# Kernel optimization log

Hardware: AMD Instinct MI355X
Metric: run time of the kernel (lower is better)

## Reference

```python
import jax, jax.numpy as jnp
import numpy as np

D = 256           # input_dim
PROCESS_STEP = 4
N_SUPPORT = 512
BATCH = 32768


def setup_inputs() -> dict:
    key = jax.random.key(0)
    ks = jax.random.split(key, 8)
    H = 2 * D  # LSTMCell hidden size
    scale = 0.05
    return {
        "support_mean": jax.random.normal(ks[0], (N_SUPPORT, D), jnp.float32),
        "support_var": jax.random.uniform(ks[1], (N_SUPPORT, D), jnp.float32),
        "query_mean": jax.random.normal(ks[2], (BATCH, D), jnp.float32),
        "query_var": jax.random.uniform(ks[3], (BATCH, D), jnp.float32),
        # LSTMCell(D, 2D) parameters (PyTorch layout: [4*H, in] / [4*H, H])
        "W_ih": jax.random.normal(ks[4], (4 * H, D), jnp.float32) * scale,
        "W_hh": jax.random.normal(ks[5], (4 * H, H), jnp.float32) * scale,
        "b_ih": jax.random.normal(ks[6], (4 * H,), jnp.float32) * scale,
        "b_hh": jax.random.normal(ks[7], (4 * H,), jnp.float32) * scale,
    }


def _lstm_cell(x, h, c, W_ih, W_hh, b_ih, b_hh):
    # gates: [B, 4H], PyTorch gate order: input, forget, cell(g), output
    gates = x @ W_ih.T + b_ih + h @ W_hh.T + b_hh
    i, f, g, o = jnp.split(gates, 4, axis=1)
    i = jax.nn.sigmoid(i)
    f = jax.nn.sigmoid(f)
    g = jnp.tanh(g)
    o = jax.nn.sigmoid(o)
    c_new = f * c + i * g
    h_new = o * jnp.tanh(c_new)
    return h_new, c_new


def reference(support_mean, support_var, query_mean, query_var,
              W_ih, W_hh, b_ih, b_hh):
    # support_var / query_var are unused by the original forward.
    B = query_mean.shape[0]
    H = 2 * D
    h_r = jnp.zeros((B, H), query_mean.dtype)
    c = jnp.zeros((B, H), query_mean.dtype)
    h = query_mean  # placeholder; overwritten in first step
    for _ in range(PROCESS_STEP):
        h_r_, c = _lstm_cell(query_mean, h_r, c, W_ih, W_hh, b_ih, b_hh)
        h = query_mean + h_r_[:, :D]                       # [B, D]
        attn = jax.nn.softmax(h @ support_mean.T, axis=1)   # [B, S]
        r = attn @ support_mean                              # [B, D]
        h_r = jnp.concatenate((h, r), axis=1)                # [B, 2D]
    matching_scores = jnp.squeeze(h @ support_mean.T)        # [B, S]
    return matching_scores
```

## Files before the change

kernel.cpp:

```cpp
#include <hip/hip_runtime.h>

typedef unsigned int uint;
typedef unsigned short ushort;
typedef __attribute__((ext_vector_type(8))) short bhalf8;
typedef __attribute__((ext_vector_type(4))) float floatx4;

#define D_IN 256
#define NUNIT 256
#define GN 1024
#define NSUP 512
#define BATCH_N 32768
#define LDA_A 768

__device__ __forceinline__ ushort f2b(float f){
  union { float f; uint u; } x; x.f = f;
  uint r = (x.u + 0x7fffu + ((x.u >> 16) & 1u)) >> 16;
  return (ushort)r;
}
__device__ __forceinline__ float b2f(ushort u){
  union { uint u; float f; } x; x.u = ((uint)u) << 16;
  return x.f;
}
__device__ __forceinline__ float sigmf(float x){ return 1.0f / (1.0f + __expf(-x)); }
__device__ __forceinline__ float tanhfast(float x){ return 1.0f - 2.0f / (1.0f + __expf(2.0f * x)); }

__device__ __forceinline__ void stage_swz4(
    ushort* lds, const ushort* __restrict__ g, int ld, int row0, int k0,
    int wave, int lane)
{
  const int rsub = lane >> 3;
  const int oct  = (lane & 7) ^ rsub;
  #pragma unroll
  for (int q = 0; q < 4; q++) {
    const ushort* gp = g + (long)(row0 + wave * 32 + q * 8 + rsub) * ld
                         + k0 + (oct << 3);
    ushort* lp = lds + (wave * 32 + q * 8) * 64;
    __builtin_amdgcn_global_load_lds(
        (const __attribute__((address_space(1))) void*)gp,
        (__attribute__((address_space(3))) void*)lp, 16, 0, 0);
  }
}

__device__ __forceinline__ void stage_swz8(
    ushort* lds, const ushort* __restrict__ g, int ld, int row0, int k0,
    int wave, int lane)
{
  const int rsub = lane >> 3;
  const int oct  = (lane & 7) ^ rsub;
  #pragma unroll
  for (int q = 0; q < 2; q++) {
    const ushort* gp = g + (long)(row0 + wave * 16 + q * 8 + rsub) * ld
                         + k0 + (oct << 3);
    ushort* lp = lds + (wave * 16 + q * 8) * 64;
    __builtin_amdgcn_global_load_lds(
        (const __attribute__((address_space(1))) void*)gp,
        (__attribute__((address_space(3))) void*)lp, 16, 0, 0);
  }
}

__device__ __forceinline__ bhalf8 frag_ld(const ushort* lds, int R, int O, int sx)
{
  return *reinterpret_cast<const bhalf8*>(&lds[R * 64 + (((O ^ sx) & 7) << 3)]);
}

__device__ __forceinline__ bhalf8 frag_ld512(const ushort* lds, int R, int g, int O, int sx)
{
  return *reinterpret_cast<const bhalf8*>(&lds[R * 512 + g * 64 + (((O ^ sx) & 7) << 3)]);
}

__global__ __launch_bounds__(512) void gemm_gq_fused(
    const ushort* __restrict__ Qb,
    const ushort* __restrict__ Wq,
    const float4* __restrict__ biasp,
    uint2* __restrict__ Gq,
    float* __restrict__ cbuf,
    const float* __restrict__ query,
    ushort* __restrict__ Hhi,
    ushort* __restrict__ Hlo)
{
  __shared__ ushort SM[2][8192];

  const int tid  = threadIdx.x;
  const int lane = tid & 63;
  const int wave = tid >> 6;
  const int wrow = (wave >> 1) * 32;
  const int wcol = (wave & 1) * 64;
  const int wg = (blockIdx.x & 7) * (gridDim.x >> 3) + (blockIdx.x >> 3);
  const int bm = wg >> 3;
  const int bn = wg & 7;
  const int rowA0 = bm * 128;
  const int colB0 = bn * 128;

  floatx4 acc[2][4];
  #pragma unroll
  for (int m = 0; m < 2; m++)
    #pragma unroll
    for (int n = 0; n < 4; n++)
      acc[m][n] = (floatx4){0.f, 0.f, 0.f, 0.f};

  const int lr = lane & 15;
  const int lg = lane >> 4;
  const int sx = lane & 7;

  for (int k0 = 0; k0 < 256; k0 += 64) {
    stage_swz8(SM[0], Qb, 256, rowA0, k0, wave, lane);
    stage_swz8(SM[1], Wq, 256, colB0, k0, wave, lane);
    __syncthreads();
    #pragma unroll
    for (int ks = 0; ks < 2; ks++) {
      bhalf8 af[2], bfr[4];
      #pragma unroll
      for (int m = 0; m < 2; m++)
        af[m] = frag_ld(SM[0], wrow + m * 16 + lr, ks * 4 + lg, sx);
      #pragma unroll
      for (int n = 0; n < 4; n++)
        bfr[n] = frag_ld(SM[1], wcol + n * 16 + lr, ks * 4 + lg, sx);
      #pragma unroll
      for (int m = 0; m < 2; m++)
        #pragma unroll
        for (int n = 0; n < 4; n++)
          acc[m][n] = __builtin_amdgcn_mfma_f32_16x16x32_bf16(af[m], bfr[n], acc[m][n], 0, 0, 0);
    }
    __syncthreads();
  }

  ushort* ehi = (ushort*)SM[0];
  ushort* elo = ehi + 128 * 32;
  float*  ec  = (float*)SM[1];

  const int u_loc = (wave & 1) * 16 + lr;
  const int u     = bn * 32 + u_loc;
  const float4 b4 = biasp[u];
  #pragma unroll
  for (int m = 0; m < 2; m++) {
    #pragma unroll
    for (int rr = 0; rr < 4; rr++) {
      const int  rloc = wrow + m * 16 + lg * 4 + rr;
      const long row  = rowA0 + rloc;
      float pi = acc[m][0][rr] + b4.x;
      float pf = acc[m][1][rr] + b4.y;
      float pg = acc[m][2][rr] + b4.z;
      float po = acc[m][3][rr] + b4.w;
      uint2 pk;
      pk.x = (uint)f2b(pi) | ((uint)f2b(pf) << 16);
      pk.y = (uint)f2b(pg) | ((uint)f2b(po) << 16);
      Gq[row * NUNIT + u] = pk;
      float cn = sigmf(pi) * tanhfast(pg);
      ec[rloc * 32 + u_loc] = cn;
      float h = query[row * D_IN + u] + sigmf(po) * tanhfast(cn);
      ushort hh = f2b(h);
      ehi[rloc * 32 + u_loc] = hh;
      elo[rloc * 32 + u_loc] = f2b(h - b2f(hh));
    }
  }
  __syncthreads();
  const int u0 = bn * 32;
  {
    int row = tid >> 2, part = tid & 3;
    *(uint4*)(Hhi + (long)(rowA0 + row) * LDA_A + u0 + part * 8) = ((const uint4*)ehi)[tid];
    *(uint4*)(Hlo + (long)(rowA0 + row) * D_IN + u0 + part * 8) = ((const uint4*)elo)[tid];
  }
  #pragma unroll
  for (int i = tid; i < 1024; i += 512) {
    int row = i >> 3, part = i & 7;
    *(uint4*)(cbuf + (long)(rowA0 + row) * NUNIT + u0 + part * 4) = ((const uint4*)ec)[i];
  }
}

__global__ __launch_bounds__(512) void gemm_gates_fused(
    const ushort* __restrict__ A,
    const ushort* __restrict__ W,
    const uint2* __restrict__ Gq,
    float* __restrict__ cbuf,
    const float* __restrict__ query,
    ushort* __restrict__ Hhi,
    ushort* __restrict__ Hlo)
{
  __shared__ ushort SM[2][2][8192];

  const int tid  = threadIdx.x;
  const int lane = tid & 63;
  const int wave = tid >> 6;
  const int wrow = (wave >> 1) * 32;
  const int wcol = (wave & 1) * 64;
  const int wg = (blockIdx.x & 7) * (gridDim.x >> 3) + (blockIdx.x >> 3);
  const int bm = wg >> 3;
  const int bn = wg & 7;
  const int rowA0 = bm * 128;
  const int colB0 = bn * 128;

  floatx4 acc[2][4];
  #pragma unroll
  for (int m = 0; m < 2; m++)
    #pragma unroll
    for (int n = 0; n < 4; n++)
      acc[m][n] = (floatx4){0.f, 0.f, 0.f, 0.f};

  const int lr = lane & 15;
  const int lg = lane >> 4;
  const int sx = lane & 7;

  stage_swz8(SM[0][0], A, LDA_A, rowA0, 0, wave, lane);
  stage_swz8(SM[0][1], W, 512,   colB0, 0, wave, lane);
  __syncthreads();

  for (int t = 0; t < 8; t++) {
    const int cur = t & 1;
    if (t + 1 < 8) {
      stage_swz8(SM[cur ^ 1][0], A, LDA_A, rowA0, (t + 1) * 64, wave, lane);
      stage_swz8(SM[cur ^ 1][1], W, 512,   colB0, (t + 1) * 64, wave, lane);
    }
    const ushort* As = SM[cur][0];
    const ushort* Bs = SM[cur][1];
    #pragma unroll
    for (int ks = 0; ks < 2; ks++) {
      bhalf8 af[2], bfr[4];
      #pragma unroll
      for (int m = 0; m < 2; m++)
        af[m] = frag_ld(As, wrow + m * 16 + lr, ks * 4 + lg, sx);
      #pragma unroll
      for (int n = 0; n < 4; n++)
        bfr[n] = frag_ld(Bs, wcol + n * 16 + lr, ks * 4 + lg, sx);
      #pragma unroll
      for (int m = 0; m < 2; m++)
        #pragma unroll
        for (int n = 0; n < 4; n++)
          acc[m][n] = __builtin_amdgcn_mfma_f32_16x16x32_bf16(af[m], bfr[n], acc[m][n], 0, 0, 0);
    }
    __syncthreads();
  }

  ushort* ehi = (ushort*)SM[0][0];
  ushort* elo = ehi + 128 * 32;
  float*  ec  = (float*)SM[0][1];

  const int u_loc = (wave & 1) * 16 + lr;
  const int u     = bn * 32 + u_loc;
  #pragma unroll
  for (int m = 0; m < 2; m++) {
    #pragma unroll
    for (int rr = 0; rr < 4; rr++) {
      const int  rloc = wrow + m * 16 + lg * 4 + rr;
      const long row  = rowA0 + rloc;
      uint2 pk = Gq[row * NUNIT + u];
      float pi = acc[m][0][rr] + b2f((ushort)(pk.x & 0xffff));
      float pf = acc[m][1][rr] + b2f((ushort)(pk.x >> 16));
      float pg = acc[m][2][rr] + b2f((ushort)(pk.y & 0xffff));
      float po = acc[m][3][rr] + b2f((ushort)(pk.y >> 16));
      float cn = sigmf(pf) * cbuf[row * NUNIT + u] + sigmf(pi) * tanhfast(pg);
      ec[rloc * 32 + u_loc] = cn;
      float h = query[row * D_IN + u] + sigmf(po) * tanhfast(cn);
      ushort hh = f2b(h);
      ehi[rloc * 32 + u_loc] = hh;
      elo[rloc * 32 + u_loc] = f2b(h - b2f(hh));
    }
  }
  __syncthreads();
  const int u0 = bn * 32;
  {
    int row = tid >> 2, part = tid & 3;
    *(uint4*)(Hhi + (long)(rowA0 + row) * LDA_A + u0 + part * 8) = ((const uint4*)ehi)[tid];
    *(uint4*)(Hlo + (long)(rowA0 + row) * D_IN + u0 + part * 8) = ((const uint4*)elo)[tid];
  }
  #pragma unroll
  for (int i = tid; i < 1024; i += 512) {
    int row = i >> 3, part = i & 7;
    *(uint4*)(cbuf + (long)(rowA0 + row) * NUNIT + u0 + part * 4) = ((const uint4*)ec)[i];
  }
}

__global__ __launch_bounds__(256) void gemm_scores(
    const ushort* __restrict__ Ahi,
    const ushort* __restrict__ Alo,
    const ushort* __restrict__ Bhi, const ushort* __restrict__ Blo,
    float* __restrict__ C)
{
  __shared__ ushort AsH[128 * 64];
  __shared__ ushort AsL[128 * 64];
  __shared__ ushort BsH[128 * 64];
  __shared__ ushort BsL[128 * 64];

  const int tid  = threadIdx.x;
  const int lane = tid & 63;
  const int wave = tid >> 6;
  const int wr = (wave >> 1) * 64;
  const int wc = (wave & 1) * 64;
  const int wg = (blockIdx.x & 7) * (gridDim.x >> 3) + (blockIdx.x >> 3);
  const int bm = wg >> 2;
  const int bn = wg & 3;
  const int rowA0 = bm * 128;
  const int rowB0 = bn * 128;

  floatx4 acc[4][4];
  #pragma unroll
  for (int m = 0; m < 4; m++)
    #pragma unroll
    for (int n = 0; n < 4; n++)
      acc[m][n] = (floatx4){0.f, 0.f, 0.f, 0.f};

  const int lr = lane & 15;
  const int lg = lane >> 4;
  const int sx = lane & 7;

  for (int k0 = 0; k0 < D_IN; k0 += 64) {
    stage_swz4(AsH, Ahi, LDA_A, rowA0, k0, wave, lane);
    stage_swz4(AsL, Alo, D_IN,  rowA0, k0, wave, lane);
    stage_swz4(BsH, Bhi, D_IN,  rowB0, k0, wave, lane);
    stage_swz4(BsL, Blo, D_IN,  rowB0, k0, wave, lane);
    __syncthreads();
    #pragma unroll
    for (int ks = 0; ks < 2; ks++) {
      bhalf8 afh[4], afl[4], bfh[4], bfl[4];
      #pragma unroll
      for (int m = 0; m < 4; m++) {
        afh[m] = frag_ld(AsH, wr + m * 16 + lr, ks * 4 + lg, sx);
        afl[m] = frag_ld(AsL, wr + m * 16 + lr, ks * 4 + lg, sx);
      }
      #pragma unroll
      for (int n = 0; n < 4; n++) {
        bfh[n] = frag_ld(BsH, wc + n * 16 + lr, ks * 4 + lg, sx);
        bfl[n] = frag_ld(BsL, wc + n * 16 + lr, ks * 4 + lg, sx);
      }
      #pragma unroll
      for (int m = 0; m < 4; m++)
        #pragma unroll
        for (int n = 0; n < 4; n++) {
          acc[m][n] = __builtin_amdgcn_mfma_f32_16x16x32_bf16(afl[m], bfh[n], acc[m][n], 0, 0, 0);
          acc[m][n] = __builtin_amdgcn_mfma_f32_16x16x32_bf16(afh[m], bfl[n], acc[m][n], 0, 0, 0);
          acc[m][n] = __builtin_amdgcn_mfma_f32_16x16x32_bf16(afh[m], bfh[n], acc[m][n], 0, 0, 0);
        }
    }
    __syncthreads();
  }

  #pragma unroll
  for (int m = 0; m < 4; m++)
    #pragma unroll
    for (int n = 0; n < 4; n++)
      #pragma unroll
      for (int r = 0; r < 4; r++) {
        int row = rowA0 + wr + m * 16 + lg * 4 + r;
        int col = rowB0 + wc + n * 16 + lr;
        C[(long)row * NSUP + col] = acc[m][n][r];
      }
}

__global__ __launch_bounds__(512) void k_spv(
    const float* __restrict__ sc,
    const ushort* __restrict__ B,
    ushort* __restrict__ Cv)
{
  __shared__ ushort Ps[32 * 512];
  __shared__ ushort Bs[256 * 64];

  const int tid  = threadIdx.x;
  const int lane = tid & 63;
  const int wave = tid >> 6;
  const int wg = (blockIdx.x & 7) * (gridDim.x >> 3) + (blockIdx.x >> 3);
  const long rowA0 = (long)wg * 32;

  const int po  = (lane >> 1) & 7;
  const int ph4 = (lane & 1) * 4;
  const int pg0 = lane >> 4;
  #pragma unroll
  for (int j = 0; j < 4; j++) {
    const int r = wave * 4 + j;
    const float4* sp = reinterpret_cast<const float4*>(sc + (rowA0 + r) * NSUP);
    float4 v0 = sp[lane];
    float4 v1 = sp[64 + lane];
    float m = fmaxf(fmaxf(fmaxf(v0.x, v0.y), fmaxf(v0.z, v0.w)),
                    fmaxf(fmaxf(v1.x, v1.y), fmaxf(v1.z, v1.w)));
    #pragma unroll
    for (int off = 32; off >= 1; off >>= 1) m = fmaxf(m, __shfl_xor(m, off));
    float e0 = __expf(v0.x - m), e1 = __expf(v0.y - m), e2 = __expf(v0.z - m), e3 = __expf(v0.w - m);
    float e4 = __expf(v1.x - m), e5 = __expf(v1.y - m), e6 = __expf(v1.z - m), e7 = __expf(v1.w - m);
    float s = e0 + e1 + e2 + e3 + e4 + e5 + e6 + e7;
    #pragma unroll
    for (int off = 32; off >= 1; off >>= 1) s += __shfl_xor(s, off);
    float inv = 1.0f / s;
    uint2 p0, p1;
    p0.x = (uint)f2b(e0 * inv) | ((uint)f2b(e1 * inv) << 16);
    p0.y = (uint)f2b(e2 * inv) | ((uint)f2b(e3 * inv) << 16);
    p1.x = (uint)f2b(e4 * inv) | ((uint)f2b(e5 * inv) << 16);
    p1.y = (uint)f2b(e6 * inv) | ((uint)f2b(e7 * inv) << 16);
    const int os = ((po ^ (r & 7)) << 3) + ph4;
    *(uint2*)&Ps[r * 512 + (pg0    ) * 64 + os] = p0;
    *(uint2*)&Ps[r * 512 + (pg0 + 4) * 64 + os] = p1;
  }
  __syncthreads();

  floatx4 acc[2][2];
  #pragma unroll
  for (int m = 0; m < 2; m++)
    #pragma unroll
    for (int n = 0; n < 2; n++)
      acc[m][n] = (floatx4){0.f, 0.f, 0.f, 0.f};

  const int lr = lane & 15;
  const int lg = lane >> 4;
  const int sx = lane & 7;

  for (int kc = 0; kc < 8; kc++) {
    stage_swz4(Bs, B, NSUP, 0, kc * 64, wave, lane);
    __syncthreads();
    #pragma unroll
    for (int ks = 0; ks < 2; ks++) {
      bhalf8 af[2], bfr[2];
      #pragma unroll
      for (int m = 0; m < 2; m++)
        af[m] = frag_ld512(Ps, m * 16 + lr, kc, ks * 4 + lg, sx);
      #pragma unroll
      for (int n = 0; n < 2; n++)
        bfr[n] = frag_ld(Bs, wave * 32 + n * 16 + lr, ks * 4 + lg, sx);
      #pragma unroll
      for (int m = 0; m < 2; m++)
        #pragma unroll
        for (int n = 0; n < 2; n++)
          acc[m][n] = __builtin_amdgcn_mfma_f32_16x16x32_bf16(af[m], bfr[n], acc[m][n], 0, 0, 0);
    }
    __syncthreads();
  }

  ushort* elr = Ps;
  #pragma unroll
  for (int m = 0; m < 2; m++)
    #pragma unroll
    for (int n = 0; n < 2; n++)
      #pragma unroll
      for (int r = 0; r < 4; r++) {
        int rloc = m * 16 + lg * 4 + r;
        int cloc = wave * 32 + n * 16 + lr;
        elr[rloc * 256 + cloc] = f2b(acc[m][n][r]);
      }
  __syncthreads();
  #pragma unroll
  for (int i = tid; i < 1024; i += 512) {
    int row = i >> 5, part = i & 31;
    *(uint4*)(Cv + (rowA0 + row) * LDA_A + part * 8) = ((const uint4*)elr)[i];
  }
}

__global__ __launch_bounds__(256) void k_build(
    const float* __restrict__ Wih, const float* __restrict__ Whh,
    const float* __restrict__ bih, const float* __restrict__ bhh,
    const float* __restrict__ S,
    ushort* __restrict__ We, ushort* __restrict__ Wo, ushort* __restrict__ Wq,
    float4* __restrict__ biasp,
    ushort* __restrict__ Shi, ushort* __restrict__ Slo,
    ushort* __restrict__ STb)
{
  int t = blockIdx.x * 256 + threadIdx.x;
  if (t < GN * 512) {
    int c = t >> 9, k = t & 511;
    int unit = (c >> 6) * 16 + (c & 15);
    int gate = (c >> 4) & 3;
    long srow = (long)(gate * 512 + unit);
    We[(long)c * 512 + k] = f2b(Whh[srow * 512 + k]);
    int ko = (k < 256) ? (256 + k) : (k - 256);
    Wo[(long)c * 512 + k] = f2b(Whh[srow * 512 + ko]);
    if (k < 256) Wq[(long)c * 256 + k] = f2b(Wih[srow * 256 + k]);
  }
  if (t < NUNIT) {
    biasp[t] = make_float4(bih[t] + bhh[t],
                           bih[512 + t] + bhh[512 + t],
                           bih[1024 + t] + bhh[1024 + t],
                           bih[1536 + t] + bhh[1536 + t]);
  }
  if (t < NSUP * D_IN) {
    float v = S[t];
    ushort hv = f2b(v);
    Shi[t] = hv;
    Slo[t] = f2b(v - b2f(hv));
    int s = t >> 8, d = t & 255;
    STb[(long)d * NSUP + s] = hv;
  }
}

__global__ __launch_bounds__(256) void k_initq(
    const float* __restrict__ query, ushort* __restrict__ Qb)
{
  long t = (long)blockIdx.x * 256 + threadIdx.x;
  Qb[t] = f2b(query[t]);
}

extern "C" void kernel_launch(void* const* d_in, const int* in_sizes, int n_in,
                              void* d_out, int out_size, void* d_ws, size_t ws_size,
                              hipStream_t stream)
{
  const float* support_mean = (const float*)d_in[0];
  const float* query_mean   = (const float*)d_in[2];
  const float* W_ih = (const float*)d_in[4];
  const float* W_hh = (const float*)d_in[5];
  const float* b_ih = (const float*)d_in[6];
  const float* b_hh = (const float*)d_in[7];
  float* out = (float*)d_out;

  char* ws = (char*)d_ws;
  size_t off = 0;
  auto alloc = [&](size_t bytes) {
    void* p = ws + off;
    off += (bytes + 255) & ~(size_t)255;
    return p;
  };
  ushort* Abuf  = (ushort*)alloc((size_t)BATCH_N * LDA_A * 2);
  ushort* Qb    = (ushort*)alloc((size_t)BATCH_N * D_IN * 2);
  ushort* We    = (ushort*)alloc((size_t)GN * 512 * 2);
  ushort* Wo    = (ushort*)alloc((size_t)GN * 512 * 2);
  ushort* Wq    = (ushort*)alloc((size_t)GN * 256 * 2);
  float4* biasp = (float4*)alloc((size_t)NUNIT * 16);
  ushort* Shi   = (ushort*)alloc((size_t)NSUP * D_IN * 2);
  ushort* Slo   = (ushort*)alloc((size_t)NSUP * D_IN * 2);
  ushort* STb   = (ushort*)alloc((size_t)D_IN * NSUP * 2);
  float*  cbuf  = (float*) alloc((size_t)BATCH_N * NUNIT * 4);
  ushort* Hlo   = (ushort*)alloc((size_t)BATCH_N * D_IN * 2);
  uint2*  Gq    = (uint2*) alloc((size_t)BATCH_N * NUNIT * 8);
  if (off > ws_size) return;

  hipLaunchKernelGGL(k_build, dim3((GN * 512) / 256), dim3(256), 0, stream,
                     W_ih, W_hh, b_ih, b_hh, support_mean,
                     We, Wo, Wq, biasp, Shi, Slo, STb);
  hipLaunchKernelGGL(k_initq, dim3((BATCH_N * D_IN) / 256), dim3(256), 0, stream,
                     query_mean, Qb);

  hipLaunchKernelGGL(gemm_gq_fused,
                     dim3((BATCH_N / 128) * (GN / 128)), dim3(512), 0, stream,
                     Qb, Wq, biasp, Gq, cbuf, query_mean, Abuf + 0, Hlo);

  for (int s = 0; s < 4; s++) {
    const int hoff = (s & 1) * 512;
    hipLaunchKernelGGL(gemm_scores,
                       dim3((BATCH_N / 128) * (NSUP / 128)), dim3(256), 0, stream,
                       Abuf + hoff, Hlo, Shi, Slo, out);
    if (s < 3) {
      hipLaunchKernelGGL(k_spv, dim3(BATCH_N / 32), dim3(512), 0, stream,
                         out, STb, Abuf + 256);
      const int aoff = ((s + 1) == 2) ? 256 : 0;
      const ushort* Wnext = ((s + 1) == 2) ? Wo : We;
      hipLaunchKernelGGL(gemm_gates_fused,
                         dim3((BATCH_N / 128) * (GN / 128)), dim3(512), 0, stream,
                         Abuf + aoff, Wnext, Gq, cbuf, query_mean,
                         Abuf + ((s + 1) & 1) * 512, Hlo);
    }
  }
}
```

Measured before the change: 499.8 us.

## Fuse score GEMM, softmax and attention-value GEMM into one kernel

Replaces the separate scores GEMM plus softmax/PV kernel in the first three steps with a single kernel. Each 64-row block computes split-precision scores against the support set in LDS, applies softmax in place, and multiplies by the transposed support matrix. This removes the fp32 score matrix round trip through global memory (32768x512 floats written and read per step) and one launch per step. In exchange, each block reloads the full support matrix from global/L2 and uses 128KB of LDS, which limits occupancy to one block per CU.

```diff
diff --git a/kernel.cpp b/kernel.cpp
--- a/kernel.cpp
+++ b/kernel.cpp
@@ -24,38 +24,35 @@
 __device__ __forceinline__ float sigmf(float x){ return 1.0f / (1.0f + __expf(-x)); }
 __device__ __forceinline__ float tanhfast(float x){ return 1.0f - 2.0f / (1.0f + __expf(2.0f * x)); }
 
+__device__ __forceinline__ void stage_rows8(
+    ushort* lds_base, const ushort* __restrict__ g, int ld,
+    long grow0, int lrow0, int k0, int lane)
+{
+  const int rsub = lane >> 3;
+  const int oct  = (lane & 7) ^ rsub;
+  const ushort* gp = g + (grow0 + lrow0 + rsub) * ld + k0 + (oct << 3);
+  ushort* lp = lds_base + lrow0 * 64;
+  __builtin_amdgcn_global_load_lds(
+      (const __attribute__((address_space(1))) void*)gp,
+      (__attribute__((address_space(3))) void*)lp, 16, 0, 0);
+}
+
 __device__ __forceinline__ void stage_swz4(
     ushort* lds, const ushort* __restrict__ g, int ld, int row0, int k0,
     int wave, int lane)
 {
-  const int rsub = lane >> 3;
-  const int oct  = (lane & 7) ^ rsub;
-  #pragma unroll
-  for (int q = 0; q < 4; q++) {
-    const ushort* gp = g + (long)(row0 + wave * 32 + q * 8 + rsub) * ld
-                         + k0 + (oct << 3);
-    ushort* lp = lds + (wave * 32 + q * 8) * 64;
-    __builtin_amdgcn_global_load_lds(
-        (const __attribute__((address_space(1))) void*)gp,
-        (__attribute__((address_space(3))) void*)lp, 16, 0, 0);
-  }
+  #pragma unroll
+  for (int q = 0; q < 4; q++)
+    stage_rows8(lds, g, ld, row0, wave * 32 + q * 8, k0, lane);
 }
 
 __device__ __forceinline__ void stage_swz8(
     ushort* lds, const ushort* __restrict__ g, int ld, int row0, int k0,
     int wave, int lane)
 {
-  const int rsub = lane >> 3;
-  const int oct  = (lane & 7) ^ rsub;
-  #pragma unroll
-  for (int q = 0; q < 2; q++) {
-    const ushort* gp = g + (long)(row0 + wave * 16 + q * 8 + rsub) * ld
-                         + k0 + (oct << 3);
-    ushort* lp = lds + (wave * 16 + q * 8) * 64;
-    __builtin_amdgcn_global_load_lds(
-        (const __attribute__((address_space(1))) void*)gp,
-        (__attribute__((address_space(3))) void*)lp, 16, 0, 0);
-  }
+  #pragma unroll
+  for (int q = 0; q < 2; q++)
+    stage_rows8(lds, g, ld, row0, wave * 16 + q * 8, k0, lane);
 }
 
 __device__ __forceinline__ bhalf8 frag_ld(const ushort* lds, int R, int O, int sx)
@@ -345,96 +342,189 @@
       }
 }
 
-__global__ __launch_bounds__(512) void k_spv(
-    const float* __restrict__ sc,
-    const ushort* __restrict__ B,
+__global__ __launch_bounds__(512) void k_sspv(
+    const ushort* __restrict__ Ahi,
+    const ushort* __restrict__ Alo,
+    const ushort* __restrict__ Shi,
+    const ushort* __restrict__ Slo,
+    const ushort* __restrict__ STb,
     ushort* __restrict__ Cv)
 {
-  __shared__ ushort Ps[32 * 512];
-  __shared__ ushort Bs[256 * 64];
+  __shared__ ushort SMEM[65536];
+  ushort* Areg = SMEM;
+  ushort* Breg = SMEM + 32768;
 
   const int tid  = threadIdx.x;
   const int lane = tid & 63;
   const int wave = tid >> 6;
   const int wg = (blockIdx.x & 7) * (gridDim.x >> 3) + (blockIdx.x >> 3);
-  const long rowA0 = (long)wg * 32;
-
+  const long rowA0 = (long)wg * 64;
+
+  const int lr = lane & 15;
+  const int lg = lane >> 4;
+  const int sx = lane & 7;
+
+  {
+    const ushort* asrc = (wave < 4) ? Ahi : Alo;
+    const int ald = (wave < 4) ? LDA_A : D_IN;
+    ushort* adst = Areg + (wave >> 2) * 16384 + (wave & 3) * 4096;
+    const int ak0 = (wave & 3) * 64;
+    #pragma unroll
+    for (int q = 0; q < 8; q++)
+      stage_rows8(adst, asrc, ald, rowA0, q * 8, ak0, lane);
+  }
+  #pragma unroll
+  for (int q = 0; q < 8; q++)
+    stage_rows8(Breg, Shi, D_IN, 0, wave * 64 + q * 8, 0, lane);
+  __syncthreads();
+
+  floatx4 acc[4][4];
+  #pragma unroll
+  for (int m = 0; m < 4; m++)
+    #pragma unroll
+    for (int n = 0; n < 4; n++)
+      acc[m][n] = (floatx4){0.f, 0.f, 0.f, 0.f};
+
+  for (int kc = 0; kc < 4; kc++) {
+    const ushort* Ah = Areg + kc * 4096;
+    const ushort* Al = Areg + 16384 + kc * 4096;
+    #pragma unroll
+    for (int ks = 0; ks < 2; ks++) {
+      bhalf8 afh[4], afl[4], bfh[4];
+      #pragma unroll
+      for (int m = 0; m < 4; m++) {
+        afh[m] = frag_ld(Ah, m * 16 + lr, ks * 4 + lg, sx);
+        afl[m] = frag_ld(Al, m * 16 + lr, ks * 4 + lg, sx);
+      }
+      #pragma unroll
+      for (int n = 0; n < 4; n++)
+        bfh[n] = frag_ld(Breg, wave * 64 + n * 16 + lr, ks * 4 + lg, sx);
+      #pragma unroll
+      for (int m = 0; m < 4; m++)
+        #pragma unroll
+        for (int n = 0; n < 4; n++) {
+          acc[m][n] = __builtin_amdgcn_mfma_f32_16x16x32_bf16(afl[m], bfh[n], acc[m][n], 0, 0, 0);
+          acc[m][n] = __builtin_amdgcn_mfma_f32_16x16x32_bf16(afh[m], bfh[n], acc[m][n], 0, 0, 0);
+        }
+    }
+    __syncthreads();
+    #pragma unroll
+    for (int q = 0; q < 8; q++)
+      stage_rows8(Breg, Slo, D_IN, 0, wave * 64 + q * 8, kc * 64, lane);
+    __syncthreads();
+    #pragma unroll
+    for (int ks = 0; ks < 2; ks++) {
+      bhalf8 afh[4], bfl[4];
+      #pragma unroll
+      for (int m = 0; m < 4; m++)
+        afh[m] = frag_ld(Ah, m * 16 + lr, ks * 4 + lg, sx);
+      #pragma unroll
+      for (int n = 0; n < 4; n++)
+        bfl[n] = frag_ld(Breg, wave * 64 + n * 16 + lr, ks * 4 + lg, sx);
+      #pragma unroll
+      for (int m = 0; m < 4; m++)
+        #pragma unroll
+        for (int n = 0; n < 4; n++)
+          acc[m][n] = __builtin_amdgcn_mfma_f32_16x16x32_bf16(afh[m], bfl[n], acc[m][n], 0, 0, 0);
+    }
+    __syncthreads();
+    if (kc < 3) {
+      #pragma unroll
+      for (int q = 0; q < 8; q++)
+        stage_rows8(Breg, Shi, D_IN, 0, wave * 64 + q * 8, (kc + 1) * 64, lane);
+      __syncthreads();
+    }
+  }
+
+  float*  scf = (float*)Breg;
+  ushort* Ps  = Areg;
   const int po  = (lane >> 1) & 7;
   const int ph4 = (lane & 1) * 4;
   const int pg0 = lane >> 4;
-  #pragma unroll
-  for (int j = 0; j < 4; j++) {
-    const int r = wave * 4 + j;
-    const float4* sp = reinterpret_cast<const float4*>(sc + (rowA0 + r) * NSUP);
-    float4 v0 = sp[lane];
-    float4 v1 = sp[64 + lane];
-    float m = fmaxf(fmaxf(fmaxf(v0.x, v0.y), fmaxf(v0.z, v0.w)),
-                    fmaxf(fmaxf(v1.x, v1.y), fmaxf(v1.z, v1.w)));
-    #pragma unroll
-    for (int off = 32; off >= 1; off >>= 1) m = fmaxf(m, __shfl_xor(m, off));
-    float e0 = __expf(v0.x - m), e1 = __expf(v0.y - m), e2 = __expf(v0.z - m), e3 = __expf(v0.w - m);
-    float e4 = __expf(v1.x - m), e5 = __expf(v1.y - m), e6 = __expf(v1.z - m), e7 = __expf(v1.w - m);
-    float s = e0 + e1 + e2 + e3 + e4 + e5 + e6 + e7;
-    #pragma unroll
-    for (int off = 32; off >= 1; off >>= 1) s += __shfl_xor(s, off);
-    float inv = 1.0f / s;
-    uint2 p0, p1;
-    p0.x = (uint)f2b(e0 * inv) | ((uint)f2b(e1 * inv) << 16);
-    p0.y = (uint)f2b(e2 * inv) | ((uint)f2b(e3 * inv) << 16);
-    p1.x = (uint)f2b(e4 * inv) | ((uint)f2b(e5 * inv) << 16);
-    p1.y = (uint)f2b(e6 * inv) | ((uint)f2b(e7 * inv) << 16);
-    const int os = ((po ^ (r & 7)) << 3) + ph4;
-    *(uint2*)&Ps[r * 512 + (pg0    ) * 64 + os] = p0;
-    *(uint2*)&Ps[r * 512 + (pg0 + 4) * 64 + os] = p1;
-  }
-  __syncthreads();
-
-  floatx4 acc[2][2];
-  #pragma unroll
-  for (int m = 0; m < 2; m++)
+
+  #pragma unroll
+  for (int half = 0; half < 2; half++) {
+    #pragma unroll
+    for (int mm = 0; mm < 2; mm++) {
+      const int m = half * 2 + mm;
+      #pragma unroll
+      for (int n = 0; n < 4; n++)
+        #pragma unroll
+        for (int r = 0; r < 4; r++)
+          scf[(mm * 16 + lg * 4 + r) * 512 + wave * 64 + n * 16 + lr] = acc[m][n][r];
+    }
+    __syncthreads();
+    #pragma unroll
+    for (int j = 0; j < 4; j++) {
+      const int rl = wave * 4 + j;
+      const int r  = half * 32 + rl;
+      const float4* sp = reinterpret_cast<const float4*>(scf + rl * 512);
+      float4 v0 = sp[lane];
+      float4 v1 = sp[64 + lane];
+      float m = fmaxf(fmaxf(fmaxf(v0.x, v0.y), fmaxf(v0.z, v0.w)),
+                      fmaxf(fmaxf(v1.x, v1.y), fmaxf(v1.z, v1.w)));
+      #pragma unroll
+      for (int off = 32; off >= 1; off >>= 1) m = fmaxf(m, __shfl_xor(m, off));
+      float e0 = __expf(v0.x - m), e1 = __expf(v0.y - m), e2 = __expf(v0.z - m), e3 = __expf(v0.w - m);
+      float e4 = __expf(v1.x - m), e5 = __expf(v1.y - m), e6 = __expf(v1.z - m), e7 = __expf(v1.w - m);
+      float s = e0 + e1 + e2 + e3 + e4 + e5 + e6 + e7;
+      #pragma unroll
+      for (int off = 32; off >= 1; off >>= 1) s += __shfl_xor(s, off);
+      float inv = 1.0f / s;
+      uint2 p0, p1;
+      p0.x = (uint)f2b(e0 * inv) | ((uint)f2b(e1 * inv) << 16);
+      p0.y = (uint)f2b(e2 * inv) | ((uint)f2b(e3 * inv) << 16);
+      p1.x = (uint)f2b(e4 * inv) | ((uint)f2b(e5 * inv) << 16);
+      p1.y = (uint)f2b(e6 * inv) | ((uint)f2b(e7 * inv) << 16);
+      const int os = ((po ^ (r & 7)) << 3) + ph4;
+      *(uint2*)&Ps[r * 512 + (pg0    ) * 64 + os] = p0;
+      *(uint2*)&Ps[r * 512 + (pg0 + 4) * 64 + os] = p1;
+    }
+    __syncthreads();
+  }
+
+  floatx4 pacc[4][2];
+  #pragma unroll
+  for (int m = 0; m < 4; m++)
     #pragma unroll
     for (int n = 0; n < 2; n++)
-      acc[m][n] = (floatx4){0.f, 0.f, 0.f, 0.f};
-
-  const int lr = lane & 15;
-  const int lg = lane >> 4;
-  const int sx = lane & 7;
-
+      pacc[m][n] = (floatx4){0.f, 0.f, 0.f, 0.f};
+
+  ushort* Bpv = Breg;
   for (int kc = 0; kc < 8; kc++) {
-    stage_swz4(Bs, B, NSUP, 0, kc * 64, wave, lane);
+    #pragma unroll
+    for (int q = 0; q < 4; q++)
+      stage_rows8(Bpv, STb, NSUP, 0, wave * 32 + q * 8, kc * 64, lane);
     __syncthreads();
     #pragma unroll
     for (int ks = 0; ks < 2; ks++) {
-      bhalf8 af[2], bfr[2];
-      #pragma unroll
-      for (int m = 0; m < 2; m++)
+      bhalf8 af[4], bfr[2];
+      #pragma unroll
+      for (int m = 0; m < 4; m++)
         af[m] = frag_ld512(Ps, m * 16 + lr, kc, ks * 4 + lg, sx);
       #pragma unroll
       for (int n = 0; n < 2; n++)
-        bfr[n] = frag_ld(Bs, wave * 32 + n * 16 + lr, ks * 4 + lg, sx);
-      #pragma unroll
-      for (int m = 0; m < 2; m++)
+        bfr[n] = frag_ld(Bpv, wave * 32 + n * 16 + lr, ks * 4 + lg, sx);
+      #pragma unroll
+      for (int m = 0; m < 4; m++)
         #pragma unroll
         for (int n = 0; n < 2; n++)
-          acc[m][n] = __builtin_amdgcn_mfma_f32_16x16x32_bf16(af[m], bfr[n], acc[m][n], 0, 0, 0);
-    }
-    __syncthreads();
-  }
-
-  ushort* elr = Ps;
-  #pragma unroll
-  for (int m = 0; m < 2; m++)
+          pacc[m][n] = __builtin_amdgcn_mfma_f32_16x16x32_bf16(af[m], bfr[n], pacc[m][n], 0, 0, 0);
+    }
+    __syncthreads();
+  }
+
+  ushort* elr = Breg + 16384;
+  #pragma unroll
+  for (int m = 0; m < 4; m++)
     #pragma unroll
     for (int n = 0; n < 2; n++)
       #pragma unroll
-      for (int r = 0; r < 4; r++) {
-        int rloc = m * 16 + lg * 4 + r;
-        int cloc = wave * 32 + n * 16 + lr;
-        elr[rloc * 256 + cloc] = f2b(acc[m][n][r]);
-      }
+      for (int r = 0; r < 4; r++)
+        elr[(m * 16 + lg * 4 + r) * 256 + wave * 32 + n * 16 + lr] = f2b(pacc[m][n][r]);
   __syncthreads();
   #pragma unroll
-  for (int i = tid; i < 1024; i += 512) {
+  for (int i = tid; i < 2048; i += 512) {
     int row = i >> 5, part = i & 31;
     *(uint4*)(Cv + (rowA0 + row) * LDA_A + part * 8) = ((const uint4*)elr)[i];
   }
@@ -526,20 +616,18 @@
                      dim3((BATCH_N / 128) * (GN / 128)), dim3(512), 0, stream,
                      Qb, Wq, biasp, Gq, cbuf, query_mean, Abuf + 0, Hlo);
 
-  for (int s = 0; s < 4; s++) {
+  for (int s = 0; s < 3; s++) {
     const int hoff = (s & 1) * 512;
-    hipLaunchKernelGGL(gemm_scores,
-                       dim3((BATCH_N / 128) * (NSUP / 128)), dim3(256), 0, stream,
-                       Abuf + hoff, Hlo, Shi, Slo, out);
-    if (s < 3) {
-      hipLaunchKernelGGL(k_spv, dim3(BATCH_N / 32), dim3(512), 0, stream,
-                         out, STb, Abuf + 256);
-      const int aoff = ((s + 1) == 2) ? 256 : 0;
-      const ushort* Wnext = ((s + 1) == 2) ? Wo : We;
-      hipLaunchKernelGGL(gemm_gates_fused,
-                         dim3((BATCH_N / 128) * (GN / 128)), dim3(512), 0, stream,
-                         Abuf + aoff, Wnext, Gq, cbuf, query_mean,
-                         Abuf + ((s + 1) & 1) * 512, Hlo);
-    }
-  }
-}
+    hipLaunchKernelGGL(k_sspv, dim3(BATCH_N / 64), dim3(512), 0, stream,
+                       Abuf + hoff, Hlo, Shi, Slo, STb, Abuf + 256);
+    const int aoff = ((s + 1) == 2) ? 256 : 0;
+    const ushort* Wnext = ((s + 1) == 2) ? Wo : We;
+    hipLaunchKernelGGL(gemm_gates_fused,
+                       dim3((BATCH_N / 128) * (GN / 128)), dim3(512), 0, stream,
+                       Abuf + aoff, Wnext, Gq, cbuf, query_mean,
+                       Abuf + ((s + 1) & 1) * 512, Hlo);
+  }
+  hipLaunchKernelGGL(gemm_scores,
+                     dim3((BATCH_N / 128) * (NSUP / 128)), dim3(256), 0, stream,
+                     Abuf + 512, Hlo, Shi, Slo, out);
+}
```

Measured after the change: 469.0 us. 1.07x faster.
